# Performance work log

Measured on AMD Instinct MI355X. Metric: run time of the kernel, lower is better.

Reference implementation:

```python
import jax, jax.numpy as jnp
import numpy as np

T = 128          # target_size
START = 126      # tag_map['start_token']
STOP = 127       # tag_map['stop_token'] == 'end_token'
NEG = -10000.0


def setup_inputs() -> dict:
    key = jax.random.key(0)
    k1, k2, k3 = jax.random.split(key, 3)
    B, S = 256, 512
    feats = jax.random.normal(k1, (B, S, T), dtype=jnp.float32)
    transitions = jax.random.normal(k2, (T, T), dtype=jnp.float32)
    # constraints from __init__: nothing transitions into start, nothing leaves end
    transitions = transitions.at[START, :].set(NEG)
    transitions = transitions.at[:, STOP].set(NEG)
    targets = jax.random.randint(k3, (B, S), 0, 126, dtype=jnp.int32)
    return {"feats": feats, "transitions": transitions, "targets": targets}


def _crf_nll(feats, transitions, targets):
    B, S, _ = feats.shape
    # ---- forward algorithm (log partition) ----
    init = jnp.full((B, T), NEG, dtype=feats.dtype).at[:, START].set(0.0)

    def step(fv, f_t):  # fv [B,T], f_t [B,T]
        # new[b, tag] = logsumexp_prev(fv[b, prev] + trans[tag, prev]) + f_t[b, tag]
        new = jax.nn.logsumexp(fv[:, None, :] + transitions[None, :, :], axis=2) + f_t
        return new, None

    fv, _ = jax.lax.scan(step, init, jnp.swapaxes(feats, 0, 1))  # scan over S
    alpha = jax.nn.logsumexp(fv + transitions[STOP][None, :], axis=1)  # [B]

    # ---- gold path score ----
    start_col = jnp.full((B, 1), START, dtype=targets.dtype)
    tags_ext = jnp.concatenate([start_col, targets], axis=1)  # [B, S+1]
    trans_score = transitions[tags_ext[:, 1:], tags_ext[:, :-1]].sum(axis=1)  # [B]
    emit_score = jnp.take_along_axis(feats, targets[..., None].astype(jnp.int32), axis=2)[..., 0].sum(axis=1)
    gold = trans_score + emit_score + transitions[STOP, tags_ext[:, -1]]  # [B]

    # module returns gold_score - alpha
    return gold - alpha


def reference(feats, transitions, targets):
    return _crf_nll(feats, transitions, targets)
```

## Files before the change

kernel.cpp:

```cpp
#include <hip/hip_runtime.h>

#define TT 128
#define SS 512
#define NB 256
#define START_TAG 126
#define STOP_TAG 127
#define NEGV -10000.0f
#define LOG2E 1.4426950408889634f
#define LN2   0.6931471805599453f

typedef float v2 __attribute__((ext_vector_type(2)));
typedef __fp16 h2 __attribute__((ext_vector_type(2)));

__device__ __forceinline__ float ex2(float x) { return __builtin_amdgcn_exp2f(x); }
__device__ __forceinline__ float lg2(float x) { return __builtin_amdgcn_logf(x); }
__device__ __forceinline__ float exn(float x) { return __builtin_amdgcn_exp2f(x * LOG2E); }

__device__ __forceinline__ float rlane(float v, int lane) {
    return __int_as_float(__builtin_amdgcn_readlane(__float_as_int(v), lane));
}
__device__ __forceinline__ int rlane_i(int v, int lane) {
    return __builtin_amdgcn_readlane(v, lane);
}
__device__ __forceinline__ float swap1(float x) {
    int i = __float_as_int(x);
    int r = __builtin_amdgcn_update_dpp(i, i, 0xB1, 0xF, 0xF, true);
    return __int_as_float(r);
}
__device__ __forceinline__ int packp(float even, float odd_src) {
    h2 h = __builtin_amdgcn_cvt_pkrtz(even, odd_src);
    return __builtin_bit_cast(int, h);
}
__device__ __forceinline__ float wave_max(float v) {
#pragma unroll
    for (int off = 32; off >= 1; off >>= 1) v = fmaxf(v, __shfl_xor(v, off));
    return v;
}
__device__ __forceinline__ float wave_sum(float v) {
#pragma unroll
    for (int off = 32; off >= 1; off >>= 1) v += __shfl_xor(v, off);
    return v;
}

#define FOR32A(M) M(0) M(1) M(2) M(3) M(4) M(5) M(6) M(7) \
  M(8) M(9) M(10) M(11) M(12) M(13) M(14) M(15) \
  M(16) M(17) M(18) M(19) M(20) M(21) M(22) M(23) \
  M(24) M(25) M(26) M(27) M(28) M(29) M(30) M(31)
#define FOR32B(M) M(32) M(33) M(34) M(35) M(36) M(37) M(38) M(39) \
  M(40) M(41) M(42) M(43) M(44) M(45) M(46) M(47) \
  M(48) M(49) M(50) M(51) M(52) M(53) M(54) M(55) \
  M(56) M(57) M(58) M(59) M(60) M(61) M(62) M(63)
#define FOR64(M) FOR32A(M) FOR32B(M)

__global__ __launch_bounds__(256, 2) void crf_fwd_kernel(
    const float* __restrict__ feats,
    const float* __restrict__ trans,
    const int*   __restrict__ targets,
    float*       __restrict__ out)
{
    const int t = threadIdx.x;
    const int b = blockIdx.x;
    const int w = t >> 6;
    const int l = t & 63;

    __shared__ v2 bshare[64];
    __shared__ float redz[4];
    __shared__ float galpha;

    const size_t bst = (size_t)b * (SS * TT);
    float statex = 0.f, statey = 0.f;

    if (w < 2) {
        const int group = w;
        const float gsel = group ? 0.f : 1.f;
        const float gnot = group ? 1.f : 0.f;

#define DECL_E(i) h2 Ex##i, Ey##i;
        FOR64(DECL_E)
#undef DECL_E

        if (group == 0) {
            const float* r0 = trans + l * TT;
            const float* r1 = trans + (l + 64) * TT;
#define INIT_FWD(i) \
            Ex##i = __builtin_amdgcn_cvt_pkrtz(exn(r0[2*(i)]), exn(r0[2*(i)+1])); \
            Ey##i = __builtin_amdgcn_cvt_pkrtz(exn(r1[2*(i)]), exn(r1[2*(i)+1]));
            FOR64(INIT_FWD)
#undef INIT_FWD
        } else {
            const float* c0 = trans + l;
            const float* c1 = trans + l + 64;
#define INIT_BWD(i) \
            Ex##i = __builtin_amdgcn_cvt_pkrtz(exn(c0[(2*(i))*TT]), exn(c0[(2*(i)+1)*TT])); \
            Ey##i = __builtin_amdgcn_cvt_pkrtz(exn(c1[(2*(i))*TT]), exn(c1[(2*(i)+1)*TT]));
            FOR64(INIT_BWD)
#undef INIT_BWD
        }

        const float* fb = feats + bst + l;

#define FIDX(i) (group ? (510 - (i)) : (i))
        float fx0 = fb[(size_t)FIDX(0) * TT] * LOG2E, fy0 = fb[(size_t)FIDX(0) * TT + 64] * LOG2E;
        float fx1 = fb[(size_t)FIDX(1) * TT] * LOG2E, fy1 = fb[(size_t)FIDX(1) * TT + 64] * LOG2E;
        float fx2 = fb[(size_t)FIDX(2) * TT] * LOG2E, fy2 = fb[(size_t)FIDX(2) * TT + 64] * LOG2E;
        float fx3 = fb[(size_t)FIDX(3) * TT] * LOG2E, fy3 = fb[(size_t)FIDX(3) * TT + 64] * LOG2E;
        const int ii = group ? 511 : 0;
        float fInx = fb[(size_t)ii * TT] * LOG2E, fIny = fb[(size_t)ii * TT + 64] * LOG2E;
#undef FIDX

        if (group == 0) {
            statex = NEGV;
            statey = (l == 62) ? 0.f : NEGV;
        } else {
            statex = trans[STOP_TAG * TT + l] * LOG2E;
            statey = trans[STOP_TAG * TT + l + 64] * LOG2E;
        }
        float agx = fmaf(fInx, gnot, statex);
        float agy = fmaf(fIny, gnot, statey);
        float M = group ? fmaxf(fmaxf(rlane(agx, 0), rlane(agy, 0)),
                                fmaxf(rlane(agx, 31), rlane(agy, 31)))
                        : 0.f;
        float px = ex2(agx - M);
        float py = ex2(agy - M);
        int ppkx = packp(px, swap1(px));
        int ppky = packp(py, swap1(py));

        for (int s = 0; s < SS / 2; ++s) {
            int sn = group ? (506 - s) : (s + 4);
            float fnx = fb[(size_t)sn * TT] * LOG2E;
            float fny = fb[(size_t)sn * TT + 64] * LOG2E;

            float accx[4] = {0.f, 0.f, 0.f, 0.f};
            float accy[4] = {0.f, 0.f, 0.f, 0.f};
#define DOTA(i) { h2 pv = __builtin_bit_cast(h2, rlane_i(ppkx, 2*(i))); \
            accx[(i)&3] = __builtin_amdgcn_fdot2(pv, Ex##i, accx[(i)&3], false); \
            accy[(i)&3] = __builtin_amdgcn_fdot2(pv, Ey##i, accy[(i)&3], false); }
            FOR32A(DOTA)
#undef DOTA
#define DOTB(i) { h2 pv = __builtin_bit_cast(h2, rlane_i(ppky, 2*(i)-64)); \
            accx[(i)&3] = __builtin_amdgcn_fdot2(pv, Ex##i, accx[(i)&3], false); \
            accy[(i)&3] = __builtin_amdgcn_fdot2(pv, Ey##i, accy[(i)&3], false); }
            FOR32B(DOTB)
#undef DOTB
            float totx = (accx[0] + accx[1]) + (accx[2] + accx[3]);
            float toty = (accy[0] + accy[1]) + (accy[2] + accy[3]);

            statex = fmaf(fx0, gsel, lg2(totx) + M);
            statey = fmaf(fy0, gsel, lg2(toty) + M);
            agx = fmaf(fx0, gnot, statex);
            agy = fmaf(fy0, gnot, statey);
            M = fmaxf(fmaxf(rlane(agx, 0), rlane(agy, 0)),
                      fmaxf(rlane(agx, 31), rlane(agy, 31)));
            px = ex2(agx - M);
            py = ex2(agy - M);
            ppkx = packp(px, swap1(px));
            ppky = packp(py, swap1(py));

            fx0 = fx1; fy0 = fy1; fx1 = fx2; fy1 = fy2;
            fx2 = fx3; fy2 = fy3; fx3 = fnx; fy3 = fny;
        }
        if (w == 1) bshare[l] = (v2){statex, statey};
    } else {
        const int* tg = targets + b * SS;
        float gs = 0.f;
        for (int i = t - 128; i < SS; i += 128) {
            int cur  = tg[i];
            int prev = (i == 0) ? START_TAG : tg[i - 1];
            gs += trans[cur * TT + prev] + feats[bst + (size_t)i * TT + cur];
        }
        if (t == 128) gs += trans[STOP_TAG * TT + tg[SS - 1]];
        gs = wave_sum(gs);
        if (l == 0) redz[w] = gs;
    }
    __syncthreads();

    if (w == 0) {
        v2 bb = bshare[l];
        float vx = statex + bb.x;
        float vy = statey + bb.y;
        float m = wave_max(fmaxf(vx, vy));
        float e = ex2(vx - m) + ex2(vy - m);
        e = wave_sum(e);
        if (l == 0) galpha = (m + lg2(e)) * LN2;
    }
    __syncthreads();

    if (t == 0) out[b] = (redz[2] + redz[3]) - galpha;
}

extern "C" void kernel_launch(void* const* d_in, const int* in_sizes, int n_in,
                              void* d_out, int out_size, void* d_ws, size_t ws_size,
                              hipStream_t stream) {
    const float* feats   = (const float*)d_in[0];
    const float* trans   = (const float*)d_in[1];
    const int*   targets = (const int*)d_in[2];
    float*       out     = (float*)d_out;
    crf_fwd_kernel<<<dim3(NB), dim3(256), 0, stream>>>(feats, trans, targets, out);
}
```

Before: 220.7 us.

## Batch CRF forward/backward chains onto MFMA with exponent-domain renormalization

Replaces the per-batch readlane/fdot2 recurrence with MFMA matrix products that process 16 sequences per wave. Scores are kept in the linear domain and rescaled each step by a power-of-two factor taken from the max exponent. A separate pre-pass exponentiates feats to fp16 in the workspace, and the gold path score is computed per block across 32 batches. This trades many parallel blocks for only 8 blocks and adds fp16 precision risk in exchange for much higher per-step throughput.

```diff
diff --git a/kernel.cpp b/kernel.cpp
--- a/kernel.cpp
+++ b/kernel.cpp
@@ -2,35 +2,22 @@
 
 #define TT 128
 #define SS 512
-#define NB 256
 #define START_TAG 126
 #define STOP_TAG 127
-#define NEGV -10000.0f
 #define LOG2E 1.4426950408889634f
 #define LN2   0.6931471805599453f
 
-typedef float v2 __attribute__((ext_vector_type(2)));
-typedef __fp16 h2 __attribute__((ext_vector_type(2)));
+typedef float f32x4 __attribute__((ext_vector_type(4)));
+typedef __fp16 f16x8 __attribute__((ext_vector_type(8)));
+typedef __fp16 h2    __attribute__((ext_vector_type(2)));
+typedef unsigned int u32;
+typedef unsigned int u32x2 __attribute__((ext_vector_type(2)));
+typedef unsigned int u32x4 __attribute__((ext_vector_type(4)));
 
 __device__ __forceinline__ float ex2(float x) { return __builtin_amdgcn_exp2f(x); }
 __device__ __forceinline__ float lg2(float x) { return __builtin_amdgcn_logf(x); }
 __device__ __forceinline__ float exn(float x) { return __builtin_amdgcn_exp2f(x * LOG2E); }
 
-__device__ __forceinline__ float rlane(float v, int lane) {
-    return __int_as_float(__builtin_amdgcn_readlane(__float_as_int(v), lane));
-}
-__device__ __forceinline__ int rlane_i(int v, int lane) {
-    return __builtin_amdgcn_readlane(v, lane);
-}
-__device__ __forceinline__ float swap1(float x) {
-    int i = __float_as_int(x);
-    int r = __builtin_amdgcn_update_dpp(i, i, 0xB1, 0xF, 0xF, true);
-    return __int_as_float(r);
-}
-__device__ __forceinline__ int packp(float even, float odd_src) {
-    h2 h = __builtin_amdgcn_cvt_pkrtz(even, odd_src);
-    return __builtin_bit_cast(int, h);
-}
 __device__ __forceinline__ float wave_max(float v) {
 #pragma unroll
     for (int off = 32; off >= 1; off >>= 1) v = fmaxf(v, __shfl_xor(v, off));
@@ -42,158 +29,261 @@
     return v;
 }
 
-#define FOR32A(M) M(0) M(1) M(2) M(3) M(4) M(5) M(6) M(7) \
-  M(8) M(9) M(10) M(11) M(12) M(13) M(14) M(15) \
-  M(16) M(17) M(18) M(19) M(20) M(21) M(22) M(23) \
-  M(24) M(25) M(26) M(27) M(28) M(29) M(30) M(31)
-#define FOR32B(M) M(32) M(33) M(34) M(35) M(36) M(37) M(38) M(39) \
-  M(40) M(41) M(42) M(43) M(44) M(45) M(46) M(47) \
-  M(48) M(49) M(50) M(51) M(52) M(53) M(54) M(55) \
-  M(56) M(57) M(58) M(59) M(60) M(61) M(62) M(63)
-#define FOR64(M) FOR32A(M) FOR32B(M)
-
-__global__ __launch_bounds__(256, 2) void crf_fwd_kernel(
+__global__ __launch_bounds__(256) void exp_feats_kernel(
+    const float* __restrict__ feats, __fp16* __restrict__ ef)
+{
+    size_t i = ((size_t)blockIdx.x * 256 + threadIdx.x) * 8;
+    f32x4 a = *(const f32x4*)(feats + i);
+    f32x4 b = *(const f32x4*)(feats + i + 4);
+    h2 r0 = __builtin_amdgcn_cvt_pkrtz(exn(a[0]), exn(a[1]));
+    h2 r1 = __builtin_amdgcn_cvt_pkrtz(exn(a[2]), exn(a[3]));
+    h2 r2 = __builtin_amdgcn_cvt_pkrtz(exn(b[0]), exn(b[1]));
+    h2 r3 = __builtin_amdgcn_cvt_pkrtz(exn(b[2]), exn(b[3]));
+    u32x4 pk;
+    pk[0] = __builtin_bit_cast(u32, r0);
+    pk[1] = __builtin_bit_cast(u32, r1);
+    pk[2] = __builtin_bit_cast(u32, r2);
+    pk[3] = __builtin_bit_cast(u32, r3);
+    *(u32x4*)(ef + i) = pk;
+}
+
+template<bool PRE>
+__device__ __forceinline__ void load_ef(const char*& pef, int sstep, u32x2 (&d)[8])
+{
+    if constexpr (PRE) {
+#pragma unroll
+        for (int tt = 0; tt < 8; ++tt) d[tt] = *(const u32x2*)(pef + 32 * tt);
+    } else {
+#pragma unroll
+        for (int tt = 0; tt < 8; ++tt) {
+            f32x4 v = *(const f32x4*)(pef + 64 * tt);
+            h2 a = __builtin_amdgcn_cvt_pkrtz(exn(v[0]), exn(v[1]));
+            h2 b = __builtin_amdgcn_cvt_pkrtz(exn(v[2]), exn(v[3]));
+            d[tt][0] = __builtin_bit_cast(u32, a);
+            d[tt][1] = __builtin_bit_cast(u32, b);
+        }
+    }
+    pef += sstep;
+}
+
+__device__ __forceinline__ void chain_step(
+    const f16x8 (&E)[8][4], f16x8 (&Bv)[4], const u32x2 (&ef)[8], int& Mint)
+{
+    const f32x4 z = {0.f, 0.f, 0.f, 0.f};
+    f32x4 a0 = __builtin_amdgcn_mfma_f32_16x16x32_f16(E[0][0], Bv[0], z, 0, 0, 0);
+    a0 = __builtin_amdgcn_mfma_f32_16x16x32_f16(E[0][1], Bv[1], a0, 0, 0, 0);
+    a0 = __builtin_amdgcn_mfma_f32_16x16x32_f16(E[0][2], Bv[2], a0, 0, 0, 0);
+    a0 = __builtin_amdgcn_mfma_f32_16x16x32_f16(E[0][3], Bv[3], a0, 0, 0, 0);
+
+    float m01 = fmaxf(fmaxf(a0[0], a0[1]), fmaxf(a0[2], a0[3]));
+    m01 = fmaxf(m01, __shfl_xor(m01, 16));
+    m01 = fmaxf(m01, __shfl_xor(m01, 32));
+    int s = ((__float_as_int(m01) >> 23) & 0xff) - 125;
+    s = s < -120 ? -120 : (s > 120 ? 120 : s);
+    Mint += s;
+    const float scf = __int_as_float((127 - s) << 23);
+
+    f32x4 acc[8];
+    acc[0] = a0;
+#pragma unroll
+    for (int tt = 1; tt < 8; ++tt)
+        acc[tt] = __builtin_amdgcn_mfma_f32_16x16x32_f16(E[tt][0], Bv[0], z, 0, 0, 0);
+#pragma unroll
+    for (int q = 1; q < 4; ++q)
+#pragma unroll
+        for (int tt = 1; tt < 8; ++tt)
+            acc[tt] = __builtin_amdgcn_mfma_f32_16x16x32_f16(E[tt][q], Bv[q], acc[tt], 0, 0, 0);
+
+    u32 pp[8][2];
+#pragma unroll
+    for (int tt = 0; tt < 8; ++tt) {
+        h2 p01 = __builtin_amdgcn_cvt_pkrtz(acc[tt][0] * scf, acc[tt][1] * scf);
+        h2 p23 = __builtin_amdgcn_cvt_pkrtz(acc[tt][2] * scf, acc[tt][3] * scf);
+        p01 *= __builtin_bit_cast(h2, ef[tt][0]);
+        p23 *= __builtin_bit_cast(h2, ef[tt][1]);
+        pp[tt][0] = __builtin_bit_cast(u32, p01);
+        pp[tt][1] = __builtin_bit_cast(u32, p23);
+    }
+#pragma unroll
+    for (int q = 0; q < 4; ++q) {
+        u32x4 bv = { pp[2 * q][0], pp[2 * q][1], pp[2 * q + 1][0], pp[2 * q + 1][1] };
+        Bv[q] = __builtin_bit_cast(f16x8, bv);
+    }
+}
+
+template<bool PRE>
+__global__ __launch_bounds__(256, 1) void crf_chain_kernel(
     const float* __restrict__ feats,
     const float* __restrict__ trans,
     const int*   __restrict__ targets,
+    const __fp16* __restrict__ efeat,
     float*       __restrict__ out)
 {
     const int t = threadIdx.x;
-    const int b = blockIdx.x;
-    const int w = t >> 6;
-    const int l = t & 63;
-
-    __shared__ v2 bshare[64];
-    __shared__ float redz[4];
-    __shared__ float galpha;
-
-    const size_t bst = (size_t)b * (SS * TT);
-    float statex = 0.f, statey = 0.f;
-
-    if (w < 2) {
-        const int group = w;
-        const float gsel = group ? 0.f : 1.f;
-        const float gnot = group ? 1.f : 0.f;
-
-#define DECL_E(i) h2 Ex##i, Ey##i;
-        FOR64(DECL_E)
-#undef DECL_E
-
-        if (group == 0) {
-            const float* r0 = trans + l * TT;
-            const float* r1 = trans + (l + 64) * TT;
-#define INIT_FWD(i) \
-            Ex##i = __builtin_amdgcn_cvt_pkrtz(exn(r0[2*(i)]), exn(r0[2*(i)+1])); \
-            Ey##i = __builtin_amdgcn_cvt_pkrtz(exn(r1[2*(i)]), exn(r1[2*(i)+1]));
-            FOR64(INIT_FWD)
-#undef INIT_FWD
-        } else {
-            const float* c0 = trans + l;
-            const float* c1 = trans + l + 64;
-#define INIT_BWD(i) \
-            Ex##i = __builtin_amdgcn_cvt_pkrtz(exn(c0[(2*(i))*TT]), exn(c0[(2*(i)+1)*TT])); \
-            Ey##i = __builtin_amdgcn_cvt_pkrtz(exn(c1[(2*(i))*TT]), exn(c1[(2*(i)+1)*TT]));
-            FOR64(INIT_BWD)
-#undef INIT_BWD
-        }
-
-        const float* fb = feats + bst + l;
-
-#define FIDX(i) (group ? (510 - (i)) : (i))
-        float fx0 = fb[(size_t)FIDX(0) * TT] * LOG2E, fy0 = fb[(size_t)FIDX(0) * TT + 64] * LOG2E;
-        float fx1 = fb[(size_t)FIDX(1) * TT] * LOG2E, fy1 = fb[(size_t)FIDX(1) * TT + 64] * LOG2E;
-        float fx2 = fb[(size_t)FIDX(2) * TT] * LOG2E, fy2 = fb[(size_t)FIDX(2) * TT + 64] * LOG2E;
-        float fx3 = fb[(size_t)FIDX(3) * TT] * LOG2E, fy3 = fb[(size_t)FIDX(3) * TT + 64] * LOG2E;
-        const int ii = group ? 511 : 0;
-        float fInx = fb[(size_t)ii * TT] * LOG2E, fIny = fb[(size_t)ii * TT + 64] * LOG2E;
-#undef FIDX
-
-        if (group == 0) {
-            statex = NEGV;
-            statey = (l == 62) ? 0.f : NEGV;
-        } else {
-            statex = trans[STOP_TAG * TT + l] * LOG2E;
-            statey = trans[STOP_TAG * TT + l + 64] * LOG2E;
-        }
-        float agx = fmaf(fInx, gnot, statex);
-        float agy = fmaf(fIny, gnot, statey);
-        float M = group ? fmaxf(fmaxf(rlane(agx, 0), rlane(agy, 0)),
-                                fmaxf(rlane(agx, 31), rlane(agy, 31)))
-                        : 0.f;
-        float px = ex2(agx - M);
-        float py = ex2(agy - M);
-        int ppkx = packp(px, swap1(px));
-        int ppky = packp(py, swap1(py));
-
-        for (int s = 0; s < SS / 2; ++s) {
-            int sn = group ? (506 - s) : (s + 4);
-            float fnx = fb[(size_t)sn * TT] * LOG2E;
-            float fny = fb[(size_t)sn * TT + 64] * LOG2E;
-
-            float accx[4] = {0.f, 0.f, 0.f, 0.f};
-            float accy[4] = {0.f, 0.f, 0.f, 0.f};
-#define DOTA(i) { h2 pv = __builtin_bit_cast(h2, rlane_i(ppkx, 2*(i))); \
-            accx[(i)&3] = __builtin_amdgcn_fdot2(pv, Ex##i, accx[(i)&3], false); \
-            accy[(i)&3] = __builtin_amdgcn_fdot2(pv, Ey##i, accy[(i)&3], false); }
-            FOR32A(DOTA)
-#undef DOTA
-#define DOTB(i) { h2 pv = __builtin_bit_cast(h2, rlane_i(ppky, 2*(i)-64)); \
-            accx[(i)&3] = __builtin_amdgcn_fdot2(pv, Ex##i, accx[(i)&3], false); \
-            accy[(i)&3] = __builtin_amdgcn_fdot2(pv, Ey##i, accy[(i)&3], false); }
-            FOR32B(DOTB)
-#undef DOTB
-            float totx = (accx[0] + accx[1]) + (accx[2] + accx[3]);
-            float toty = (accy[0] + accy[1]) + (accy[2] + accy[3]);
-
-            statex = fmaf(fx0, gsel, lg2(totx) + M);
-            statey = fmaf(fy0, gsel, lg2(toty) + M);
-            agx = fmaf(fx0, gnot, statex);
-            agy = fmaf(fy0, gnot, statey);
-            M = fmaxf(fmaxf(rlane(agx, 0), rlane(agy, 0)),
-                      fmaxf(rlane(agx, 31), rlane(agy, 31)));
-            px = ex2(agx - M);
-            py = ex2(agy - M);
-            ppkx = packp(px, swap1(px));
-            ppky = packp(py, swap1(py));
-
-            fx0 = fx1; fy0 = fy1; fx1 = fx2; fy1 = fy2;
-            fx2 = fx3; fy2 = fy3; fx3 = fnx; fy3 = fny;
-        }
-        if (w == 1) bshare[l] = (v2){statex, statey};
+    const int w = t >> 6, l = t & 63;
+    const int c = l & 15, h = l >> 4;
+    const int base = blockIdx.x * 32;
+    const int bb = (w & 1) * 16 + c;
+    const int batch = base + bb;
+    const bool isFwd = (w >> 1) == 0;
+    const int side = isFwd ? 0 : 1;
+
+    __shared__ __align__(16) float AB[2][32][TT];
+    __shared__ float salpha[32];
+    __shared__ float gpart[32][8];
+
+    f16x8 E[8][4];
+#pragma unroll
+    for (int tt = 0; tt < 8; ++tt) {
+        const int ro = 16 * tt + c;
+#pragma unroll
+        for (int q = 0; q < 4; ++q) {
+            f16x8 F;
+            if (isFwd) {
+                f32x4 t0 = *(const f32x4*)(trans + ro * TT + 32 * q + 4 * h);
+                f32x4 t1 = *(const f32x4*)(trans + ro * TT + 32 * q + 16 + 4 * h);
+#pragma unroll
+                for (int j = 0; j < 4; ++j) {
+                    F[j]     = (__fp16)exn(t0[j]);
+                    F[j + 4] = (__fp16)exn(t1[j]);
+                }
+            } else {
+#pragma unroll
+                for (int j = 0; j < 8; ++j) {
+                    const int k = 32 * q + ((j & 4) << 2) + 4 * h + (j & 3);
+                    F[j] = (__fp16)exn(trans[k * TT + ro]);
+                }
+            }
+            E[tt][q] = F;
+        }
+    }
+
+    f16x8 Bv[4];
+#pragma unroll
+    for (int q = 0; q < 4; ++q) {
+#pragma unroll
+        for (int j = 0; j < 8; ++j) {
+            const int k = 32 * q + ((j & 4) << 2) + 4 * h + (j & 3);
+            float v;
+            if (isFwd) v = (k == START_TAG) ? 1.f : 0.f;
+            else       v = exn(trans[STOP_TAG * TT + k] +
+                               feats[((size_t)batch * SS + 511) * TT + k]);
+            Bv[q][j] = (__fp16)v;
+        }
+    }
+
+    const char* pef;
+    int sstep;
+    if constexpr (PRE) {
+        pef = (const char*)efeat + 2 * (((size_t)batch * SS + (isFwd ? 0 : 510)) * TT) + 8 * h;
+        sstep = isFwd ? (TT * 2) : -(TT * 2);
     } else {
-        const int* tg = targets + b * SS;
+        pef = (const char*)feats + 4 * (((size_t)batch * SS + (isFwd ? 0 : 510)) * TT) + 16 * h;
+        sstep = isFwd ? (TT * 4) : -(TT * 4);
+    }
+
+    int Mint = 0;
+    u32x2 e0[8], e1[8], e2[8], e3[8];
+    load_ef<PRE>(pef, sstep, e0);
+    load_ef<PRE>(pef, sstep, e1);
+    load_ef<PRE>(pef, sstep, e2);
+    load_ef<PRE>(pef, sstep, e3);
+#pragma unroll 1
+    for (int it = 0; it < 62; ++it) {
+        chain_step(E, Bv, e0, Mint); load_ef<PRE>(pef, sstep, e0);
+        chain_step(E, Bv, e1, Mint); load_ef<PRE>(pef, sstep, e1);
+        chain_step(E, Bv, e2, Mint); load_ef<PRE>(pef, sstep, e2);
+        chain_step(E, Bv, e3, Mint); load_ef<PRE>(pef, sstep, e3);
+    }
+    chain_step(E, Bv, e0, Mint); load_ef<PRE>(pef, sstep, e0);
+    chain_step(E, Bv, e1, Mint); load_ef<PRE>(pef, sstep, e1);
+    chain_step(E, Bv, e2, Mint); load_ef<PRE>(pef, sstep, e2);
+    chain_step(E, Bv, e3, Mint); load_ef<PRE>(pef, sstep, e3);
+    chain_step(E, Bv, e0, Mint);
+    chain_step(E, Bv, e1, Mint);
+    chain_step(E, Bv, e2, Mint);
+
+    const f32x4 z = {0.f, 0.f, 0.f, 0.f};
+    f32x4 acc[8];
+#pragma unroll
+    for (int tt = 0; tt < 8; ++tt)
+        acc[tt] = __builtin_amdgcn_mfma_f32_16x16x32_f16(E[tt][0], Bv[0], z, 0, 0, 0);
+#pragma unroll
+    for (int q = 1; q < 4; ++q)
+#pragma unroll
+        for (int tt = 0; tt < 8; ++tt)
+            acc[tt] = __builtin_amdgcn_mfma_f32_16x16x32_f16(E[tt][q], Bv[q], acc[tt], 0, 0, 0);
+
+    const float Mtotf = (float)Mint;
+#pragma unroll
+    for (int tt = 0; tt < 8; ++tt) {
+        float ev0 = 1.f, ev1 = 1.f, ev2 = 1.f, ev3 = 1.f;
+        if (isFwd) {
+            h2 a = __builtin_bit_cast(h2, e3[tt][0]);
+            h2 b = __builtin_bit_cast(h2, e3[tt][1]);
+            ev0 = (float)a[0]; ev1 = (float)a[1]; ev2 = (float)b[0]; ev3 = (float)b[1];
+        }
+        f32x4 v;
+        v[0] = Mtotf + lg2(fmaxf(acc[tt][0] * ev0, 1e-35f));
+        v[1] = Mtotf + lg2(fmaxf(acc[tt][1] * ev1, 1e-35f));
+        v[2] = Mtotf + lg2(fmaxf(acc[tt][2] * ev2, 1e-35f));
+        v[3] = Mtotf + lg2(fmaxf(acc[tt][3] * ev3, 1e-35f));
+        *(f32x4*)&AB[side][bb][16 * tt + 4 * h] = v;
+    }
+    __syncthreads();
+
+#pragma unroll 1
+    for (int k8 = 0; k8 < 8; ++k8) {
+        const int bq = w * 8 + k8;
+        float v0 = AB[0][bq][l] + AB[1][bq][l];
+        float v1 = AB[0][bq][l + 64] + AB[1][bq][l + 64];
+        float mm = wave_max(fmaxf(v0, v1));
+        float ss = wave_sum(ex2(v0 - mm) + ex2(v1 - mm));
+        if (l == 0) salpha[bq] = (mm + lg2(ss)) * LN2;
+    }
+
+    {
+        const int bbg = t & 31, ck = t >> 5;
+        const int gb  = base + bbg;
+        const int* tg = targets + gb * SS;
+        const float* fb = feats + (size_t)gb * SS * TT;
         float gs = 0.f;
-        for (int i = t - 128; i < SS; i += 128) {
-            int cur  = tg[i];
-            int prev = (i == 0) ? START_TAG : tg[i - 1];
-            gs += trans[cur * TT + prev] + feats[bst + (size_t)i * TT + cur];
-        }
-        if (t == 128) gs += trans[STOP_TAG * TT + tg[SS - 1]];
-        gs = wave_sum(gs);
-        if (l == 0) redz[w] = gs;
+        const int i0 = ck * 64;
+        int prev = (i0 == 0) ? START_TAG : tg[i0 - 1];
+        for (int i = i0; i < i0 + 64; ++i) {
+            int cur = tg[i];
+            gs += trans[cur * TT + prev] + fb[(size_t)i * TT + cur];
+            prev = cur;
+        }
+        if (ck == 7) gs += trans[STOP_TAG * TT + tg[SS - 1]];
+        gpart[bbg][ck] = gs;
     }
     __syncthreads();
 
-    if (w == 0) {
-        v2 bb = bshare[l];
-        float vx = statex + bb.x;
-        float vy = statey + bb.y;
-        float m = wave_max(fmaxf(vx, vy));
-        float e = ex2(vx - m) + ex2(vy - m);
-        e = wave_sum(e);
-        if (l == 0) galpha = (m + lg2(e)) * LN2;
-    }
-    __syncthreads();
-
-    if (t == 0) out[b] = (redz[2] + redz[3]) - galpha;
+    if (t < 32) {
+        float g = 0.f;
+#pragma unroll
+        for (int k = 0; k < 8; ++k) g += gpart[t][k];
+        out[base + t] = g - salpha[t];
+    }
 }
 
 extern "C" void kernel_launch(void* const* d_in, const int* in_sizes, int n_in,
                               void* d_out, int out_size, void* d_ws, size_t ws_size,
                               hipStream_t stream) {
+    (void)in_sizes; (void)n_in; (void)out_size;
     const float* feats   = (const float*)d_in[0];
     const float* trans   = (const float*)d_in[1];
     const int*   targets = (const int*)d_in[2];
     float*       out     = (float*)d_out;
-    crf_fwd_kernel<<<dim3(NB), dim3(256), 0, stream>>>(feats, trans, targets, out);
-}
+
+    const size_t efbytes = (size_t)256 * SS * TT * sizeof(__fp16);
+    if (d_ws && ws_size >= efbytes) {
+        __fp16* ef = (__fp16*)d_ws;
+        exp_feats_kernel<<<dim3(8192), dim3(256), 0, stream>>>(feats, ef);
+        crf_chain_kernel<true><<<dim3(8), dim3(256), 0, stream>>>(feats, trans, targets, ef, out);
+    } else {
+        crf_chain_kernel<false><<<dim3(8), dim3(256), 0, stream>>>(feats, trans, targets,
+                                                                   (const __fp16*)nullptr, out);
+    }
+}
```

Result: slower. 385.6 us (+74.7%).
